# Performance work log

Measured on AMD Instinct MI355X. Metric: run time of the kernel, lower is better.

The kernel has to match this reference:

```python
import jax, jax.numpy as jnp
import numpy as np


def _conv(x, w):
    # stride-2, pad-1, 3x3 conv, NCHW activations, HWIO kernel
    return jax.lax.conv_general_dilated(
        x, w, (2, 2), [(1, 1), (1, 1)],
        dimension_numbers=('NCHW', 'HWIO', 'NCHW'))


def setup_inputs() -> dict:
    key = jax.random.key(0)
    ks = iter(jax.random.split(key, 40))
    def rn(shape, scale=1.0):
        return jax.random.normal(next(ks), shape, jnp.float32) * scale
    d = {}
    d['img'] = rn((64, 3, 128, 128))
    d['qst'] = rn((64, 128))
    d['conv_w0'] = rn((3, 3, 3, 24), 1.0 / np.sqrt(3 * 9))
    for i in (1, 2, 3):
        d['conv_w%d' % i] = rn((3, 3, 24, 24), 1.0 / np.sqrt(24 * 9))
    for i in range(4):
        d['bn_s%d' % i] = jax.random.uniform(next(ks), (24,), jnp.float32, 0.5, 1.5)
        d['bn_b%d' % i] = rn((24,), 0.1)
    d['g_w1'] = rn((180, 256), 1.0 / np.sqrt(180))
    d['g_b1'] = rn((256,), 0.01)
    for i in (2, 3, 4):
        d['g_w%d' % i] = rn((256, 256), 1.0 / np.sqrt(256))
        d['g_b%d' % i] = rn((256,), 0.01)
    d['f_w1'] = rn((256, 256), 1.0 / np.sqrt(256))
    d['f_b1'] = rn((256,), 0.01)
    d['f_w2'] = rn((256, 256), 1.0 / np.sqrt(256))
    d['f_b2'] = rn((256,), 0.01)
    d['cls_w'] = rn((256, 32), 1.0 / np.sqrt(256))
    d['cls_b'] = rn((32,), 0.01)
    return d


def reference(img, qst, conv_w0, conv_w1, conv_w2, conv_w3,
              bn_s0, bn_b0, bn_s1, bn_b1, bn_s2, bn_b2, bn_s3, bn_b3,
              g_w1, g_b1, g_w2, g_b2, g_w3, g_b3, g_w4, g_b4,
              f_w1, f_b1, f_w2, f_b2, cls_w, cls_b):
    x = img
    for w, s, b in ((conv_w0, bn_s0, bn_b0), (conv_w1, bn_s1, bn_b1),
                    (conv_w2, bn_s2, bn_b2), (conv_w3, bn_s3, bn_b3)):
        x = jax.nn.relu(_conv(x, w) * s[None, :, None, None] + b[None, :, None, None])
    N, C, H, W = x.shape  # [64, 24, 8, 8]
    # positional encoding: coords_x, coords_y in [-1,1]
    cx, cy = jnp.meshgrid(jnp.linspace(-1.0, 1.0, W), jnp.linspace(-1.0, 1.0, H))
    pos = jnp.broadcast_to(jnp.stack([cx, cy])[None], (N, 2, H, W)).astype(x.dtype)
    x = jnp.concatenate([x, pos], axis=1)              # [N, C+2, H, W]
    Cf = C + 2
    x = x.transpose(0, 2, 3, 1).reshape(N, H * W, Cf)  # [N, HW, 26]
    # RN_G first linear decomposed over concat([x_i, x_j, qst]) so the huge
    # [N, HW, HW, 2C+q] concat tensor is never materialized (same math).
    W1a, W1b, W1c = g_w1[:Cf], g_w1[Cf:2 * Cf], g_w1[2 * Cf:]
    hi = x @ W1a                      # [N, HW, 256]
    hj = x @ W1b                      # [N, HW, 256]
    hq = qst @ W1c + g_b1             # [N, 256]
    h = jax.nn.relu(hi[:, :, None, :] + hj[:, None, :, :] + hq[:, None, None, :])  # [N,HW,HW,256]
    h = jax.nn.relu(h @ g_w2 + g_b2)
    h = jax.nn.relu(h @ g_w3 + g_b3)
    h = jax.nn.relu(h @ g_w4 + g_b4)
    s = h.sum(axis=(1, 2))            # sum over all HW*HW pairs -> [N, 256]
    # RN_F (dropout is identity in eval mode)
    y = jax.nn.relu(s @ f_w1 + f_b1)
    y = jax.nn.relu(y @ f_w2 + f_b2)
    return jax.nn.log_softmax(y @ cls_w + cls_b, axis=1)
```

## Files before the change

kernel.cpp:

```cpp
#include <hip/hip_runtime.h>
#include <hip/hip_bf16.h>
#include <math.h>

typedef __bf16 bf16x8 __attribute__((ext_vector_type(8)));
typedef __bf16 bf16x4 __attribute__((ext_vector_type(4)));
typedef float  f32x4  __attribute__((ext_vector_type(4)));

#define LH 264

__device__ __host__ inline int fperm(int p) {
  return (p & 0xC0) | ((p & 0x0C) << 2) | ((p >> 2) & 0x0C) | (p & 3);
}

__global__ __launch_bounds__(256) void k1(const float* __restrict__ img, const float* __restrict__ w0,
    const float* __restrict__ bs0, const float* __restrict__ bb0,
    const float* __restrict__ g2, const float* __restrict__ g3, const float* __restrict__ g4,
    const float* __restrict__ gw1, const float* __restrict__ gb1, const float* __restrict__ qst,
    float* __restrict__ c0, __bf16* __restrict__ Wt, float* __restrict__ hq,
    float* __restrict__ sbuf) {
  __shared__ __align__(16) float smem[8224];
  const int blk = blockIdx.x, t = threadIdx.x;

  if (blk < 512) {
    float* wl = smem;
    for (int i = t; i < 648; i += 256) wl[i] = w0[i];
    __syncthreads();
    const int H = 128, W = 128, OH = 64, OW = 64;
    int idx = blk * 256 + t;
    int oxh = idx & 31; int tt = idx >> 5; int oy = tt & 63; int n = tt >> 6;
    int ox0 = oxh * 2;
    float acc0[24], acc1[24];
#pragma unroll
    for (int co = 0; co < 24; ++co) { acc0[co] = 0.f; acc1[co] = 0.f; }
    for (int ci = 0; ci < 3; ++ci) {
      const float* xp = img + (size_t)(n * 3 + ci) * H * W;
#pragma unroll
      for (int ky = 0; ky < 3; ++ky) {
        int iy = 2 * oy + ky - 1;
        if (iy < 0 || iy >= H) continue;
        const float* row = xp + (size_t)iy * W;
        int ixb = 2 * ox0 - 1;
        float in[7];
#pragma unroll
        for (int u = 0; u < 7; ++u) {
          int ix = ixb + u;
          in[u] = (ix >= 0 && ix < W) ? row[ix] : 0.f;
        }
#pragma unroll
        for (int kx = 0; kx < 3; ++kx) {
          const float* wp = &wl[((ky * 3 + kx) * 3 + ci) * 24];
          float v0 = in[kx], v1 = in[kx + 2];
#pragma unroll
          for (int co = 0; co < 24; ++co) {
            float wv = wp[co];
            acc0[co] += v0 * wv;
            acc1[co] += v1 * wv;
          }
        }
      }
    }
    float* yp = c0 + (size_t)n * 24 * OH * OW + (size_t)oy * OW + ox0;
#pragma unroll
    for (int co = 0; co < 24; ++co) {
      float s = bs0[co], b = bb0[co];
      yp[(size_t)co * OH * OW]     = fmaxf(acc0[co] * s + b, 0.f);
      yp[(size_t)co * OH * OW + 1] = fmaxf(acc1[co] * s + b, 0.f);
    }
  } else if (blk < 536) {
    float* tile = smem;
    const int lb = blk - 512;
    const int l = lb >> 3, ks = lb & 7;
    const float* src = (l == 0) ? g2 : (l == 1) ? g3 : g4;
    for (int kk = 0; kk < 32; ++kk) tile[kk * 257 + t] = src[(ks * 32 + kk) * 256 + t];
    __syncthreads();
    const int q = t & 3, nb = t >> 2;
    __bf16* out = Wt + (size_t)(l * 8 + ks) * 8192;
#pragma unroll
    for (int i = 0; i < 4; ++i) {
      int nn = i * 64 + nb;
      int fsel = (l < 2) ? fperm(nn) : nn;
      bf16x8 v;
#pragma unroll
      for (int j = 0; j < 8; ++j) v[j] = (__bf16)tile[(q * 8 + j) * 257 + fsel];
      *(bf16x8*)&out[nn * 32 + q * 8] = v;
    }
  } else {
    float* qs = smem;
    const int n = blk - 536;
    sbuf[n * 256 + t] = 0.f;
    if (t < 128) qs[t] = qst[n * 128 + t];
    __syncthreads();
    float a = gb1[t];
    for (int c = 0; c < 128; ++c) a += qs[c] * gw1[(52 + c) * 256 + t];
    hq[n * 256 + t] = a;
  }
}

__global__ __launch_bounds__(256) void conv1_k(const float* __restrict__ x, const float* __restrict__ w,
                                               const float* __restrict__ sc, const float* __restrict__ bi,
                                               float* __restrict__ y) {
  const int H = 64, W = 64, OH = 32, OW = 32;
  __shared__ float wl[2592];
  const int half = blockIdx.x & 1, sb = blockIdx.x >> 1;
  for (int i = threadIdx.x; i < 2592; i += 256) {
    int co = i % 12, rest = i / 12;
    wl[i] = w[rest * 24 + half * 12 + co];
  }
  __syncthreads();

  int idx = sb * 256 + threadIdx.x;
  int oxh = idx & 15; int tt = idx >> 4; int oy = tt & 31; int n = tt >> 5;
  int ox0 = oxh * 2;

  float acc0[12], acc1[12];
#pragma unroll
  for (int co = 0; co < 12; ++co) { acc0[co] = 0.f; acc1[co] = 0.f; }

  for (int ci = 0; ci < 24; ++ci) {
    const float* xp = x + (size_t)(n * 24 + ci) * H * W;
#pragma unroll
    for (int ky = 0; ky < 3; ++ky) {
      int iy = 2 * oy + ky - 1;
      if (iy < 0 || iy >= H) continue;
      const float* row = xp + (size_t)iy * W;
      int ixb = 2 * ox0 - 1;
      float in[7];
#pragma unroll
      for (int u = 0; u < 7; ++u) {
        int ix = ixb + u;
        in[u] = (ix >= 0 && ix < W) ? row[ix] : 0.f;
      }
#pragma unroll
      for (int kx = 0; kx < 3; ++kx) {
        const float* wp = &wl[((ky * 3 + kx) * 24 + ci) * 12];
        float v0 = in[kx], v1 = in[kx + 2];
#pragma unroll
        for (int co = 0; co < 12; ++co) {
          float wv = wp[co];
          acc0[co] += v0 * wv;
          acc1[co] += v1 * wv;
        }
      }
    }
  }
  float* yp = y + (size_t)n * 24 * OH * OW + (size_t)(half * 12) * OH * OW + (size_t)oy * OW + ox0;
#pragma unroll
  for (int co = 0; co < 12; ++co) {
    int cog = half * 12 + co;
    float s = sc[cog], b = bi[cog];
    yp[(size_t)co * OH * OW]     = fmaxf(acc0[co] * s + b, 0.f);
    yp[(size_t)co * OH * OW + 1] = fmaxf(acc1[co] * s + b, 0.f);
  }
}

__global__ __launch_bounds__(256) void chain2_k(const float* __restrict__ c1,
    const float* __restrict__ w2, const float* __restrict__ bs2, const float* __restrict__ bb2,
    const float* __restrict__ w3, const float* __restrict__ bs3, const float* __restrict__ bb3,
    const float* __restrict__ gw1, float* __restrict__ hi, float* __restrict__ hj) {
  __shared__ float sw[5184];
  __shared__ float s2[6144];
  __shared__ float s3[1536];
  const int n = blockIdx.x, t = threadIdx.x;
  for (int i = t; i < 5184; i += 256) sw[i] = w2[i];
  __syncthreads();
  {
    int ox = t & 15, oy = t >> 4;
    float acc[24];
#pragma unroll
    for (int co = 0; co < 24; ++co) acc[co] = 0.f;
    for (int ci = 0; ci < 24; ++ci) {
      const float* xp = c1 + (size_t)(n * 24 + ci) * 1024;
#pragma unroll
      for (int ky = 0; ky < 3; ++ky) {
        int iy = 2 * oy + ky - 1;
        if (iy < 0 || iy >= 32) continue;
#pragma unroll
        for (int kx = 0; kx < 3; ++kx) {
          int ix = 2 * ox + kx - 1;
          if (ix < 0 || ix >= 32) continue;
          float v = xp[iy * 32 + ix];
          const float* wp = &sw[((ky * 3 + kx) * 24 + ci) * 24];
#pragma unroll
          for (int co = 0; co < 24; ++co) acc[co] += v * wp[co];
        }
      }
    }
#pragma unroll
    for (int co = 0; co < 24; ++co)
      s2[co * 256 + t] = fmaxf(acc[co] * bs2[co] + bb2[co], 0.f);
  }
  __syncthreads();
  for (int i = t; i < 5184; i += 256) sw[i] = w3[i];
  __syncthreads();
  {
    const int pos = t & 63, cog = t >> 6;
    const int oy = pos >> 3, ox = pos & 7;
    float acc[6];
#pragma unroll
    for (int u = 0; u < 6; ++u) acc[u] = 0.f;
    for (int ci = 0; ci < 24; ++ci) {
      const float* cp = &s2[ci * 256];
#pragma unroll
      for (int ky = 0; ky < 3; ++ky) {
        int iy = 2 * oy + ky - 1;
        if (iy < 0 || iy >= 16) continue;
#pragma unroll
        for (int kx = 0; kx < 3; ++kx) {
          int ix = 2 * ox + kx - 1;
          if (ix < 0 || ix >= 16) continue;
          float v = cp[iy * 16 + ix];
          const float* wp = &sw[((ky * 3 + kx) * 24 + ci) * 24 + cog * 6];
#pragma unroll
          for (int u = 0; u < 6; ++u) acc[u] += v * wp[u];
        }
      }
    }
#pragma unroll
    for (int u = 0; u < 6; ++u) {
      int co = cog * 6 + u;
      s3[co * 64 + pos] = fmaxf(acc[u] * bs3[co] + bb3[co], 0.f);
    }
  }
  float wa[26], wb[26];
#pragma unroll
  for (int c = 0; c < 26; ++c) {
    wa[c] = gw1[c * 256 + t];
    wb[c] = gw1[(26 + c) * 256 + t];
  }
  __syncthreads();
  for (int p = 0; p < 64; ++p) {
    float a = 0.f, b = 0.f;
#pragma unroll
    for (int c = 0; c < 24; ++c) {
      float v = s3[c * 64 + p];
      a += v * wa[c];
      b += v * wb[c];
    }
    float cx = -1.f + (2.f / 7.f) * (float)(p & 7);
    float cy = -1.f + (2.f / 7.f) * (float)(p >> 3);
    a += cx * wa[24] + cy * wa[25];
    b += cx * wb[24] + cy * wb[25];
    hi[(size_t)(n * 64 + p) * 256 + t] = a;
    hj[(size_t)(n * 64 + p) * 256 + t] = b;
  }
}

__global__ __launch_bounds__(256, 2)
void g_fused(const float* __restrict__ hi, const float* __restrict__ hj,
             const float* __restrict__ hq, const __bf16* __restrict__ Wt,
             const float* __restrict__ b2, const float* __restrict__ b3,
             const float* __restrict__ b4, float* __restrict__ s_out) {
  const int blk = blockIdx.x;
  const int n = blk >> 5, ib = blk & 31;
  const int tid = threadIdx.x;
  const int wave = tid >> 6, lane = tid & 63;
  const int q = lane >> 4, lr = lane & 15;

  __shared__ __align__(16) __bf16 Hs[128 * LH];

  const int half = lane >> 5, m = lane & 31;
  const int cb = m * 8;
  float4 hqA = *(const float4*)(hq + (size_t)n * 256 + cb);
  float4 hqB = *(const float4*)(hq + (size_t)n * 256 + cb + 4);
  float4 hiA = *(const float4*)(hi + (size_t)(n * 64 + ib * 2 + half) * 256 + cb);
  float4 hiB = *(const float4*)(hi + (size_t)(n * 64 + ib * 2 + half) * 256 + cb + 4);
  float hh[8];
  hh[0] = hiA.x + hqA.x; hh[1] = hiA.y + hqA.y; hh[2] = hiA.z + hqA.z; hh[3] = hiA.w + hqA.w;
  hh[4] = hiB.x + hqB.x; hh[5] = hiB.y + hqB.y; hh[6] = hiB.z + hqB.z; hh[7] = hiB.w + hqB.w;

  float bias2[4];
#pragma unroll
  for (int c = 0; c < 4; ++c) bias2[c] = b4[wave * 64 + lr + c * 16];

  const float* hjb = hj + (size_t)n * 64 * 256;
#pragma unroll
  for (int it = 0; it < 16; ++it) {
    int j = it * 4 + wave;
    float4 va = *(const float4*)(hjb + j * 256 + cb);
    float4 vb = *(const float4*)(hjb + j * 256 + cb + 4);
    bf16x8 o;
    o[0] = (__bf16)fmaxf(va.x + hh[0], 0.f);
    o[1] = (__bf16)fmaxf(va.y + hh[1], 0.f);
    o[2] = (__bf16)fmaxf(va.z + hh[2], 0.f);
    o[3] = (__bf16)fmaxf(va.w + hh[3], 0.f);
    o[4] = (__bf16)fmaxf(vb.x + hh[4], 0.f);
    o[5] = (__bf16)fmaxf(vb.y + hh[5], 0.f);
    o[6] = (__bf16)fmaxf(vb.z + hh[6], 0.f);
    o[7] = (__bf16)fmaxf(vb.w + hh[7], 0.f);
    *(bf16x8*)&Hs[(size_t)(half * 64 + j) * LH + cb] = o;
  }
  __syncthreads();

  const __bf16* Bp = Wt + (size_t)wave * 2048 + lr * 32 + q * 8;
  const int colv = wave * 64 + q * 16;

  for (int l = 0; l < 2; ++l) {
    const __bf16* Bl = Bp + (size_t)l * 65536;
    const float* bb = (l == 0) ? b2 : b3;
    f32x4 bv[4];
#pragma unroll
    for (int c = 0; c < 4; ++c)
      bv[c] = *(const f32x4*)(bb + colv + c * 4);

    f32x4 acc[8][4];
#pragma unroll
    for (int r = 0; r < 8; ++r)
#pragma unroll
      for (int c = 0; c < 4; ++c) acc[r][c] = (f32x4){0.f, 0.f, 0.f, 0.f};

    for (int ks = 0; ks < 8; ++ks) {
      bf16x8 b[4];
#pragma unroll
      for (int c = 0; c < 4; ++c)
        b[c] = *(const bf16x8*)&Bl[ks * 8192 + c * 512];
      bf16x8 a[8];
#pragma unroll
      for (int r = 0; r < 8; ++r)
        a[r] = *(const bf16x8*)&Hs[(size_t)(r * 16 + lr) * LH + ks * 32 + q * 8];
#pragma unroll
      for (int r = 0; r < 8; ++r)
#pragma unroll
        for (int c = 0; c < 4; ++c)
          acc[r][c] = __builtin_amdgcn_mfma_f32_16x16x32_bf16(b[c], a[r], acc[r][c], 0, 0, 0);
    }

    __syncthreads();
#pragma unroll
    for (int r = 0; r < 8; ++r) {
      bf16x8 oA, oB;
#pragma unroll
      for (int c = 0; c < 2; ++c)
#pragma unroll
        for (int reg = 0; reg < 4; ++reg)
          oA[c * 4 + reg] = (__bf16)fmaxf(acc[r][c][reg] + bv[c][reg], 0.f);
#pragma unroll
      for (int c = 2; c < 4; ++c)
#pragma unroll
        for (int reg = 0; reg < 4; ++reg)
          oB[(c - 2) * 4 + reg] = (__bf16)fmaxf(acc[r][c][reg] + bv[c][reg], 0.f);
      __bf16* wp = &Hs[(size_t)(r * 16 + lr) * LH + colv];
      *(bf16x8*)wp = oA;
      *(bf16x8*)(wp + 8) = oB;
    }
    __syncthreads();
  }

  {
    const __bf16* Bl = Bp + (size_t)2 * 65536;
    f32x4 acc[8][4];
#pragma unroll
    for (int r = 0; r < 8; ++r)
#pragma unroll
      for (int c = 0; c < 4; ++c) acc[r][c] = (f32x4){0.f, 0.f, 0.f, 0.f};

    for (int ks = 0; ks < 8; ++ks) {
      bf16x8 b[4];
#pragma unroll
      for (int c = 0; c < 4; ++c)
        b[c] = *(const bf16x8*)&Bl[ks * 8192 + c * 512];
      bf16x8 a[8];
#pragma unroll
      for (int r = 0; r < 8; ++r)
        a[r] = *(const bf16x8*)&Hs[(size_t)(r * 16 + lr) * LH + ks * 32 + q * 8];
#pragma unroll
      for (int r = 0; r < 8; ++r)
#pragma unroll
        for (int c = 0; c < 4; ++c)
          acc[r][c] = __builtin_amdgcn_mfma_f32_16x16x32_bf16(a[r], b[c], acc[r][c], 0, 0, 0);
    }

#pragma unroll
    for (int c = 0; c < 4; ++c) {
      float cs = 0.f;
#pragma unroll
      for (int r = 0; r < 8; ++r)
#pragma unroll
        for (int reg = 0; reg < 4; ++reg)
          cs += fmaxf(acc[r][c][reg] + bias2[c], 0.f);
      cs += __shfl_xor(cs, 16);
      cs += __shfl_xor(cs, 32);
      if (q == 0) atomicAdd(&s_out[n * 256 + wave * 64 + lr + c * 16], cs);
    }
  }
}

__global__ void f_net(const float* __restrict__ s, const float* __restrict__ fw1,
                      const float* __restrict__ fb1, const float* __restrict__ fw2,
                      const float* __restrict__ fb2, const float* __restrict__ cw,
                      const float* __restrict__ cb, float* __restrict__ out) {
  int n = blockIdx.x, t = threadIdx.x;
  __shared__ float buf[256], buf2[256], zs[32];
  buf[t] = s[n * 256 + t];
  __syncthreads();
  float a = fb1[t];
  for (int c = 0; c < 256; ++c) a += buf[c] * fw1[c * 256 + t];
  a = fmaxf(a, 0.f);
  buf2[t] = a;
  __syncthreads();
  float y = fb2[t];
  for (int c = 0; c < 256; ++c) y += buf2[c] * fw2[c * 256 + t];
  y = fmaxf(y, 0.f);
  __syncthreads();
  buf[t] = y;
  __syncthreads();
  float z = 0.f;
  if (t < 32) {
    z = cb[t];
    for (int c = 0; c < 256; ++c) z += buf[c] * cw[c * 32 + t];
    zs[t] = z;
  }
  __syncthreads();
  if (t < 32) {
    float m = -1e30f;
    for (int c = 0; c < 32; ++c) m = fmaxf(m, zs[c]);
    float se = 0.f;
    for (int c = 0; c < 32; ++c) se += expf(zs[c] - m);
    out[n * 32 + t] = z - m - logf(se);
  }
}

extern "C" void kernel_launch(void* const* d_in, const int* in_sizes, int n_in,
                              void* d_out, int out_size, void* d_ws, size_t ws_size,
                              hipStream_t stream) {
  const float* img  = (const float*)d_in[0];
  const float* qst  = (const float*)d_in[1];
  const float* w0   = (const float*)d_in[2];
  const float* w1   = (const float*)d_in[3];
  const float* w2   = (const float*)d_in[4];
  const float* w3   = (const float*)d_in[5];
  const float* bs0  = (const float*)d_in[6];
  const float* bb0  = (const float*)d_in[7];
  const float* bs1  = (const float*)d_in[8];
  const float* bb1  = (const float*)d_in[9];
  const float* bs2  = (const float*)d_in[10];
  const float* bb2  = (const float*)d_in[11];
  const float* bs3  = (const float*)d_in[12];
  const float* bb3  = (const float*)d_in[13];
  const float* gw1  = (const float*)d_in[14];
  const float* gb1  = (const float*)d_in[15];
  const float* gw2  = (const float*)d_in[16];
  const float* gb2  = (const float*)d_in[17];
  const float* gw3  = (const float*)d_in[18];
  const float* gb3  = (const float*)d_in[19];
  const float* gw4  = (const float*)d_in[20];
  const float* gb4  = (const float*)d_in[21];
  const float* fw1  = (const float*)d_in[22];
  const float* fb1  = (const float*)d_in[23];
  const float* fw2  = (const float*)d_in[24];
  const float* fb2  = (const float*)d_in[25];
  const float* cw   = (const float*)d_in[26];
  const float* cb   = (const float*)d_in[27];

  char* ws = (char*)d_ws;
  float* c0 = (float*)(ws + 0);
  float* c1 = (float*)(ws + 25165824);
  __bf16* Wt  = (__bf16*)(ws + 31457280);
  float*  hqb = (float*)(ws + 31850496);
  float*  sbuf = (float*)(ws + 31916032);
  float*  hi  = (float*)(ws + 0);
  float*  hj  = (float*)(ws + 4194304);

  k1<<<600, 256, 0, stream>>>(img, w0, bs0, bb0, gw2, gw3, gw4, gw1, gb1, qst,
                              c0, Wt, hqb, sbuf);
  conv1_k<<<256, 256, 0, stream>>>(c0, w1, bs1, bb1, c1);
  chain2_k<<<64, 256, 0, stream>>>(c1, w2, bs2, bb2, w3, bs3, bb3, gw1, hi, hj);
  g_fused<<<2048, 256, 0, stream>>>(hi, hj, hqb, Wt, gb2, gb3, gb4, sbuf);
  f_net<<<64, 256, 0, stream>>>(sbuf, fw1, fb1, fw2, fb2, cw, cb, (float*)d_out);
}
```

Baseline: 308.9 us.

## Switch conv activations to NHWC, split embedding into separate kernel, unroll f_net

Conv0 and conv1 now write channels-last activations with float4 stores, and conv1 and conv2 read them as contiguous channel vectors. Conv1 now has each thread compute all 24 output channels for one pixel instead of half the channels for two pixels, with the full weight set in shared memory. The per-position hi/hj embedding is split out of the 64-block chain2 kernel into a new 256-block kernel to spread that work, at the cost of an extra launch and a global round-trip through a workspace buffer. f_net's dot products use four independent accumulators to shorten dependency chains.

```diff
diff --git a/kernel.cpp b/kernel.cpp
--- a/kernel.cpp
+++ b/kernel.cpp
@@ -25,7 +25,7 @@
     float* wl = smem;
     for (int i = t; i < 648; i += 256) wl[i] = w0[i];
     __syncthreads();
-    const int H = 128, W = 128, OH = 64, OW = 64;
+    const int H = 128, W = 128;
     int idx = blk * 256 + t;
     int oxh = idx & 31; int tt = idx >> 5; int oy = tt & 63; int n = tt >> 6;
     int ox0 = oxh * 2;
@@ -59,12 +59,26 @@
         }
       }
     }
-    float* yp = c0 + (size_t)n * 24 * OH * OW + (size_t)oy * OW + ox0;
-#pragma unroll
-    for (int co = 0; co < 24; ++co) {
-      float s = bs0[co], b = bb0[co];
-      yp[(size_t)co * OH * OW]     = fmaxf(acc0[co] * s + b, 0.f);
-      yp[(size_t)co * OH * OW + 1] = fmaxf(acc1[co] * s + b, 0.f);
+    float* yp = c0 + ((size_t)((n * 64 + oy) * 64) + ox0) * 24;
+#pragma unroll
+    for (int v = 0; v < 6; ++v) {
+      f32x4 o;
+#pragma unroll
+      for (int j = 0; j < 4; ++j) {
+        int co = v * 4 + j;
+        o[j] = fmaxf(acc0[co] * bs0[co] + bb0[co], 0.f);
+      }
+      *(f32x4*)(yp + v * 4) = o;
+    }
+#pragma unroll
+    for (int v = 0; v < 6; ++v) {
+      f32x4 o;
+#pragma unroll
+      for (int j = 0; j < 4; ++j) {
+        int co = v * 4 + j;
+        o[j] = fmaxf(acc1[co] * bs0[co] + bb0[co], 0.f);
+      }
+      *(f32x4*)(yp + 24 + v * 4) = o;
     }
   } else if (blk < 536) {
     float* tile = smem;
@@ -99,95 +113,97 @@
 __global__ __launch_bounds__(256) void conv1_k(const float* __restrict__ x, const float* __restrict__ w,
                                                const float* __restrict__ sc, const float* __restrict__ bi,
                                                float* __restrict__ y) {
-  const int H = 64, W = 64, OH = 32, OW = 32;
-  __shared__ float wl[2592];
-  const int half = blockIdx.x & 1, sb = blockIdx.x >> 1;
-  for (int i = threadIdx.x; i < 2592; i += 256) {
-    int co = i % 12, rest = i / 12;
-    wl[i] = w[rest * 24 + half * 12 + co];
-  }
-  __syncthreads();
-
-  int idx = sb * 256 + threadIdx.x;
-  int oxh = idx & 15; int tt = idx >> 4; int oy = tt & 31; int n = tt >> 5;
-  int ox0 = oxh * 2;
-
-  float acc0[12], acc1[12];
-#pragma unroll
-  for (int co = 0; co < 12; ++co) { acc0[co] = 0.f; acc1[co] = 0.f; }
-
-  for (int ci = 0; ci < 24; ++ci) {
-    const float* xp = x + (size_t)(n * 24 + ci) * H * W;
-#pragma unroll
-    for (int ky = 0; ky < 3; ++ky) {
-      int iy = 2 * oy + ky - 1;
-      if (iy < 0 || iy >= H) continue;
-      const float* row = xp + (size_t)iy * W;
-      int ixb = 2 * ox0 - 1;
-      float in[7];
-#pragma unroll
-      for (int u = 0; u < 7; ++u) {
-        int ix = ixb + u;
-        in[u] = (ix >= 0 && ix < W) ? row[ix] : 0.f;
-      }
-#pragma unroll
-      for (int kx = 0; kx < 3; ++kx) {
-        const float* wp = &wl[((ky * 3 + kx) * 24 + ci) * 12];
-        float v0 = in[kx], v1 = in[kx + 2];
-#pragma unroll
-        for (int co = 0; co < 12; ++co) {
-          float wv = wp[co];
-          acc0[co] += v0 * wv;
-          acc1[co] += v1 * wv;
+  __shared__ __align__(16) float wl[5184];
+  const int t = threadIdx.x;
+  for (int i = t; i < 5184; i += 256) wl[i] = w[i];
+  __syncthreads();
+  int idx = blockIdx.x * 256 + t;
+  int ox = idx & 31, oy = (idx >> 5) & 31, n = idx >> 10;
+  f32x4 acc4[6];
+#pragma unroll
+  for (int v = 0; v < 6; ++v) acc4[v] = (f32x4){0.f, 0.f, 0.f, 0.f};
+  const float* xb = x + (size_t)n * 4096 * 24;
+#pragma unroll
+  for (int ky = 0; ky < 3; ++ky) {
+    int iy = 2 * oy + ky - 1;
+    if (iy < 0 || iy >= 64) continue;
+#pragma unroll
+    for (int kx = 0; kx < 3; ++kx) {
+      int ix = 2 * ox + kx - 1;
+      if (ix < 0 || ix >= 64) continue;
+      const float* xp = xb + (size_t)(iy * 64 + ix) * 24;
+      const float* wt = &wl[((ky * 3 + kx) * 24) * 24];
+      for (int c4 = 0; c4 < 6; ++c4) {
+        f32x4 xq = *(const f32x4*)(xp + c4 * 4);
+        const float* wb4 = wt + (c4 * 4) * 24;
+#pragma unroll
+        for (int j = 0; j < 4; ++j) {
+          float v = xq[j];
+          const f32x4* wr = (const f32x4*)(wb4 + j * 24);
+#pragma unroll
+          for (int cv = 0; cv < 6; ++cv) acc4[cv] += v * wr[cv];
         }
       }
     }
   }
-  float* yp = y + (size_t)n * 24 * OH * OW + (size_t)(half * 12) * OH * OW + (size_t)oy * OW + ox0;
-#pragma unroll
-  for (int co = 0; co < 12; ++co) {
-    int cog = half * 12 + co;
-    float s = sc[cog], b = bi[cog];
-    yp[(size_t)co * OH * OW]     = fmaxf(acc0[co] * s + b, 0.f);
-    yp[(size_t)co * OH * OW + 1] = fmaxf(acc1[co] * s + b, 0.f);
+  float* yp = y + (size_t)idx * 24;
+#pragma unroll
+  for (int v = 0; v < 6; ++v) {
+    f32x4 o;
+#pragma unroll
+    for (int j = 0; j < 4; ++j) {
+      int co = v * 4 + j;
+      o[j] = fmaxf(acc4[v][j] * sc[co] + bi[co], 0.f);
+    }
+    *(f32x4*)(yp + v * 4) = o;
   }
 }
 
 __global__ __launch_bounds__(256) void chain2_k(const float* __restrict__ c1,
     const float* __restrict__ w2, const float* __restrict__ bs2, const float* __restrict__ bb2,
     const float* __restrict__ w3, const float* __restrict__ bs3, const float* __restrict__ bb3,
-    const float* __restrict__ gw1, float* __restrict__ hi, float* __restrict__ hj) {
-  __shared__ float sw[5184];
+    float* __restrict__ gs3) {
+  __shared__ __align__(16) float sw[5184];
   __shared__ float s2[6144];
-  __shared__ float s3[1536];
   const int n = blockIdx.x, t = threadIdx.x;
   for (int i = t; i < 5184; i += 256) sw[i] = w2[i];
   __syncthreads();
   {
     int ox = t & 15, oy = t >> 4;
-    float acc[24];
-#pragma unroll
-    for (int co = 0; co < 24; ++co) acc[co] = 0.f;
-    for (int ci = 0; ci < 24; ++ci) {
-      const float* xp = c1 + (size_t)(n * 24 + ci) * 1024;
-#pragma unroll
-      for (int ky = 0; ky < 3; ++ky) {
-        int iy = 2 * oy + ky - 1;
-        if (iy < 0 || iy >= 32) continue;
-#pragma unroll
-        for (int kx = 0; kx < 3; ++kx) {
-          int ix = 2 * ox + kx - 1;
-          if (ix < 0 || ix >= 32) continue;
-          float v = xp[iy * 32 + ix];
-          const float* wp = &sw[((ky * 3 + kx) * 24 + ci) * 24];
-#pragma unroll
-          for (int co = 0; co < 24; ++co) acc[co] += v * wp[co];
+    f32x4 acc4[6];
+#pragma unroll
+    for (int v = 0; v < 6; ++v) acc4[v] = (f32x4){0.f, 0.f, 0.f, 0.f};
+    const float* xb = c1 + (size_t)n * 1024 * 24;
+#pragma unroll
+    for (int ky = 0; ky < 3; ++ky) {
+      int iy = 2 * oy + ky - 1;
+      if (iy < 0 || iy >= 32) continue;
+#pragma unroll
+      for (int kx = 0; kx < 3; ++kx) {
+        int ix = 2 * ox + kx - 1;
+        if (ix < 0 || ix >= 32) continue;
+        const float* xp = xb + (size_t)(iy * 32 + ix) * 24;
+        const float* wt = &sw[((ky * 3 + kx) * 24) * 24];
+        for (int c4 = 0; c4 < 6; ++c4) {
+          f32x4 xq = *(const f32x4*)(xp + c4 * 4);
+          const float* wb4 = wt + (c4 * 4) * 24;
+#pragma unroll
+          for (int j = 0; j < 4; ++j) {
+            float v = xq[j];
+            const f32x4* wr = (const f32x4*)(wb4 + j * 24);
+#pragma unroll
+            for (int cv = 0; cv < 6; ++cv) acc4[cv] += v * wr[cv];
+          }
         }
       }
     }
 #pragma unroll
-    for (int co = 0; co < 24; ++co)
-      s2[co * 256 + t] = fmaxf(acc[co] * bs2[co] + bb2[co], 0.f);
+    for (int v = 0; v < 6; ++v)
+#pragma unroll
+      for (int j = 0; j < 4; ++j) {
+        int co = v * 4 + j;
+        s2[co * 256 + t] = fmaxf(acc4[v][j] * bs2[co] + bb2[co], 0.f);
+      }
   }
   __syncthreads();
   for (int i = t; i < 5184; i += 256) sw[i] = w3[i];
@@ -218,9 +234,17 @@
 #pragma unroll
     for (int u = 0; u < 6; ++u) {
       int co = cog * 6 + u;
-      s3[co * 64 + pos] = fmaxf(acc[u] * bs3[co] + bb3[co], 0.f);
-    }
-  }
+      gs3[(size_t)n * 1536 + co * 64 + pos] = fmaxf(acc[u] * bs3[co] + bb3[co], 0.f);
+    }
+  }
+}
+
+__global__ __launch_bounds__(256) void embed_k(const float* __restrict__ gs3,
+    const float* __restrict__ gw1, float* __restrict__ hi, float* __restrict__ hj) {
+  __shared__ float s3l[1536];
+  const int b = blockIdx.x, t = threadIdx.x;
+  const int n = b >> 2, pg = b & 3;
+  for (int i = t; i < 1536; i += 256) s3l[i] = gs3[(size_t)n * 1536 + i];
   float wa[26], wb[26];
 #pragma unroll
   for (int c = 0; c < 26; ++c) {
@@ -228,20 +252,20 @@
     wb[c] = gw1[(26 + c) * 256 + t];
   }
   __syncthreads();
-  for (int p = 0; p < 64; ++p) {
-    float a = 0.f, b = 0.f;
+  for (int p = pg * 16; p < pg * 16 + 16; ++p) {
+    float a = 0.f, bv = 0.f;
 #pragma unroll
     for (int c = 0; c < 24; ++c) {
-      float v = s3[c * 64 + p];
+      float v = s3l[c * 64 + p];
       a += v * wa[c];
-      b += v * wb[c];
+      bv += v * wb[c];
     }
     float cx = -1.f + (2.f / 7.f) * (float)(p & 7);
     float cy = -1.f + (2.f / 7.f) * (float)(p >> 3);
     a += cx * wa[24] + cy * wa[25];
-    b += cx * wb[24] + cy * wb[25];
+    bv += cx * wb[24] + cy * wb[25];
     hi[(size_t)(n * 64 + p) * 256 + t] = a;
-    hj[(size_t)(n * 64 + p) * 256 + t] = b;
+    hj[(size_t)(n * 64 + p) * 256 + t] = bv;
   }
 }
 
@@ -392,21 +416,37 @@
   __shared__ float buf[256], buf2[256], zs[32];
   buf[t] = s[n * 256 + t];
   __syncthreads();
-  float a = fb1[t];
-  for (int c = 0; c < 256; ++c) a += buf[c] * fw1[c * 256 + t];
-  a = fmaxf(a, 0.f);
+  float a0 = 0.f, a1 = 0.f, a2 = 0.f, a3 = 0.f;
+  for (int c = 0; c < 256; c += 4) {
+    a0 += buf[c]     * fw1[c * 256 + t];
+    a1 += buf[c + 1] * fw1[(c + 1) * 256 + t];
+    a2 += buf[c + 2] * fw1[(c + 2) * 256 + t];
+    a3 += buf[c + 3] * fw1[(c + 3) * 256 + t];
+  }
+  float a = fmaxf(fb1[t] + ((a0 + a1) + (a2 + a3)), 0.f);
   buf2[t] = a;
   __syncthreads();
-  float y = fb2[t];
-  for (int c = 0; c < 256; ++c) y += buf2[c] * fw2[c * 256 + t];
-  y = fmaxf(y, 0.f);
+  float y0 = 0.f, y1 = 0.f, y2 = 0.f, y3 = 0.f;
+  for (int c = 0; c < 256; c += 4) {
+    y0 += buf2[c]     * fw2[c * 256 + t];
+    y1 += buf2[c + 1] * fw2[(c + 1) * 256 + t];
+    y2 += buf2[c + 2] * fw2[(c + 2) * 256 + t];
+    y3 += buf2[c + 3] * fw2[(c + 3) * 256 + t];
+  }
+  float y = fmaxf(fb2[t] + ((y0 + y1) + (y2 + y3)), 0.f);
   __syncthreads();
   buf[t] = y;
   __syncthreads();
   float z = 0.f;
   if (t < 32) {
-    z = cb[t];
-    for (int c = 0; c < 256; ++c) z += buf[c] * cw[c * 32 + t];
+    float z0 = 0.f, z1 = 0.f, z2 = 0.f, z3 = 0.f;
+    for (int c = 0; c < 256; c += 4) {
+      z0 += buf[c]     * cw[c * 32 + t];
+      z1 += buf[c + 1] * cw[(c + 1) * 32 + t];
+      z2 += buf[c + 2] * cw[(c + 2) * 32 + t];
+      z3 += buf[c + 3] * cw[(c + 3) * 32 + t];
+    }
+    z = cb[t] + ((z0 + z1) + (z2 + z3));
     zs[t] = z;
   }
   __syncthreads();
@@ -459,11 +499,13 @@
   float*  sbuf = (float*)(ws + 31916032);
   float*  hi  = (float*)(ws + 0);
   float*  hj  = (float*)(ws + 4194304);
+  float*  gs3 = (float*)(ws + 8388608);
 
   k1<<<600, 256, 0, stream>>>(img, w0, bs0, bb0, gw2, gw3, gw4, gw1, gb1, qst,
                               c0, Wt, hqb, sbuf);
   conv1_k<<<256, 256, 0, stream>>>(c0, w1, bs1, bb1, c1);
-  chain2_k<<<64, 256, 0, stream>>>(c1, w2, bs2, bb2, w3, bs3, bb3, gw1, hi, hj);
+  chain2_k<<<64, 256, 0, stream>>>(c1, w2, bs2, bb2, w3, bs3, bb3, gs3);
+  embed_k<<<256, 256, 0, stream>>>(gs3, gw1, hi, hj);
   g_fused<<<2048, 256, 0, stream>>>(hi, hj, hqb, Wt, gb2, gb3, gb4, sbuf);
   f_net<<<64, 256, 0, stream>>>(sbuf, fw1, fb1, fw2, fb2, cw, cb, (float*)d_out);
 }
```

After: 313.6 us. About the same (+1.5%).
